# Kernel tuning notes

Hardware: AMD Instinct MI355X
Metric: run time of the kernel (lower is better)

The kernel has to match this reference:

```python
import jax, jax.numpy as jnp
import numpy as np

HID = 1024      # hidden_size (embedding dim, GRU input)
RNN = 1024      # rnn_hidden_size
VOCAB = 50000   # max_node
STEPS = 1024    # num_steps
SOS = 0


def setup_inputs() -> dict:
    key = jax.random.key(0)
    ks = jax.random.split(key, 8)
    s = 0.02
    return {
        "inputs": jax.random.randint(ks[0], (STEPS,), 0, VOCAB),
        "z": jax.random.normal(ks[1], (RNN,), jnp.float32),
        "emb_W": jax.random.uniform(ks[2], (VOCAB, HID), jnp.float32, -0.001, 0.001),
        "out_b": jnp.full((VOCAB,), 0.01, jnp.float32),
        "h2e_W": jax.random.normal(ks[3], (HID, RNN), jnp.float32) * s,
        "h2e_b": jnp.full((HID,), 0.01, jnp.float32),
        "W_ih": jax.random.normal(ks[4], (3 * RNN, HID), jnp.float32) * s,
        "W_hh": jax.random.normal(ks[5], (3 * RNN, RNN), jnp.float32) * s,
        "b_ih": jnp.zeros((3 * RNN,), jnp.float32),
        "b_hh": jnp.zeros((3 * RNN,), jnp.float32),
    }


def reference(inputs, z, emb_W, out_b, h2e_W, h2e_b, W_ih, W_hh, b_ih, b_hh):
    R = RNN

    def gru_cell(h, x):
        gi = W_ih @ x + b_ih          # (3R,)
        gh = W_hh @ h + b_hh          # (3R,)
        r = jax.nn.sigmoid(gi[:R] + gh[:R])
        zg = jax.nn.sigmoid(gi[R:2 * R] + gh[R:2 * R])
        n = jnp.tanh(gi[2 * R:] + r * gh[2 * R:])
        return (1.0 - zg) * n + zg * h

    # teacher forcing: step i consumes token_{i-1} (SOS for i=1), target is inputs[i]
    step_tokens = jnp.concatenate([jnp.array([SOS], dtype=inputs.dtype), inputs[1:-1]])
    targets = inputs[1:]

    def step(h, tok_tgt):
        tok, tgt = tok_tgt
        x = emb_W[tok]                              # embedding lookup (HID,)
        h_new = gru_cell(h, x)                      # (RNN,)
        e = h2e_W @ h_new + h2e_b                   # (HID,)
        logp = jax.nn.log_softmax(emb_W @ e + out_b)  # tied weights, (VOCAB,)
        return h_new, (-logp[tgt], jnp.argmax(logp))

    _, (losses, preds) = jax.lax.scan(step, z, (step_tokens, targets))
    loss = jnp.sum(losses)
    outputs = jnp.zeros((1, inputs.shape[0]), dtype=jnp.int32).at[0, 1:].set(preds.astype(jnp.int32))
    return loss, outputs
```

## Files before the change

kernel.cpp:

```cpp
#include <hip/hip_runtime.h>
#include <math.h>

#define NV      50000
#define T_STEPS 1023
#define KDIM    1024
#define NCH     782
typedef unsigned long long ull;


__global__ __launch_bounds__(256) void k_gather(const int* __restrict__ inputs,
                                                const float* __restrict__ emb,
                                                float* __restrict__ X) {
  const int t = blockIdx.x;
  const int tid = threadIdx.x;
  float4 v = make_float4(0.f, 0.f, 0.f, 0.f);
  if (t < T_STEPS) {
    const int tok = (t == 0) ? 0 : inputs[t];
    v = *(const float4*)&emb[(size_t)tok * KDIM + tid * 4];
  }
  *(float4*)&X[(size_t)t * KDIM + tid * 4] = v;
}

__global__ __launch_bounds__(256) void k_gemm_ffd(const float* __restrict__ A,
                                                  const float* __restrict__ B,
                                                  const float* __restrict__ bias,
                                                  double* __restrict__ C,
                                                  int N, int K) {
  __shared__ float As[32][68];
  __shared__ float Bs[32][68];
  const int tid = threadIdx.x;
  const int bx = blockIdx.x, by = blockIdx.y;
  const int lr = tid >> 2;
  const int lk = (tid & 3) * 8;
  const float* Ap = A + (size_t)(by * 64 + lr) * K + lk;
  const float* Bp = B + (size_t)(bx * 64 + lr) * K + lk;
  const int r0 = (tid >> 4) * 4;
  const int c0 = (tid & 15) * 4;
  double acc[4][4] = {};
  for (int kc = 0; kc < K; kc += 32) {
    const float4 a0 = *(const float4*)(Ap + kc);
    const float4 a1 = *(const float4*)(Ap + kc + 4);
    const float4 b0 = *(const float4*)(Bp + kc);
    const float4 b1 = *(const float4*)(Bp + kc + 4);
    __syncthreads();
    As[lk+0][lr]=a0.x; As[lk+1][lr]=a0.y; As[lk+2][lr]=a0.z; As[lk+3][lr]=a0.w;
    As[lk+4][lr]=a1.x; As[lk+5][lr]=a1.y; As[lk+6][lr]=a1.z; As[lk+7][lr]=a1.w;
    Bs[lk+0][lr]=b0.x; Bs[lk+1][lr]=b0.y; Bs[lk+2][lr]=b0.z; Bs[lk+3][lr]=b0.w;
    Bs[lk+4][lr]=b1.x; Bs[lk+5][lr]=b1.y; Bs[lk+6][lr]=b1.z; Bs[lk+7][lr]=b1.w;
    __syncthreads();
#pragma unroll
    for (int kk = 0; kk < 32; ++kk) {
      const float4 av = *(const float4*)&As[kk][r0];
      const float4 bv = *(const float4*)&Bs[kk][c0];
      const double aa[4] = {av.x, av.y, av.z, av.w};
      const double bb[4] = {bv.x, bv.y, bv.z, bv.w};
#pragma unroll
      for (int i = 0; i < 4; ++i)
#pragma unroll
        for (int j = 0; j < 4; ++j)
          acc[i][j] = fma(aa[i], bb[j], acc[i][j]);
    }
  }
  const int row = by * 64 + r0;
  const int col = bx * 64 + c0;
#pragma unroll
  for (int i = 0; i < 4; ++i)
#pragma unroll
    for (int j = 0; j < 4; ++j)
      C[(size_t)(row + i) * N + col + j] = acc[i][j] + (double)bias[col + j];
}

__global__ __launch_bounds__(256) void k_gemm_dfd(const double* __restrict__ A,
                                                  const float* __restrict__ B,
                                                  const float* __restrict__ bias,
                                                  double* __restrict__ C,
                                                  int N, int K) {
  __shared__ double As[32][68];
  __shared__ float  Bs[32][68];
  const int tid = threadIdx.x;
  const int bx = blockIdx.x, by = blockIdx.y;
  const int lr = tid >> 2;
  const int lk = (tid & 3) * 8;
  const double* Ap = A + (size_t)(by * 64 + lr) * K + lk;
  const float*  Bp = B + (size_t)(bx * 64 + lr) * K + lk;
  const int r0 = (tid >> 4) * 4;
  const int c0 = (tid & 15) * 4;
  double acc[4][4] = {};
  for (int kc = 0; kc < K; kc += 32) {
    double ar[8];
#pragma unroll
    for (int q = 0; q < 8; ++q) ar[q] = Ap[kc + q];
    const float4 b0 = *(const float4*)(Bp + kc);
    const float4 b1 = *(const float4*)(Bp + kc + 4);
    __syncthreads();
#pragma unroll
    for (int q = 0; q < 8; ++q) As[lk + q][lr] = ar[q];
    Bs[lk+0][lr]=b0.x; Bs[lk+1][lr]=b0.y; Bs[lk+2][lr]=b0.z; Bs[lk+3][lr]=b0.w;
    Bs[lk+4][lr]=b1.x; Bs[lk+5][lr]=b1.y; Bs[lk+6][lr]=b1.z; Bs[lk+7][lr]=b1.w;
    __syncthreads();
#pragma unroll
    for (int kk = 0; kk < 32; ++kk) {
      const double aa[4] = {As[kk][r0+0], As[kk][r0+1], As[kk][r0+2], As[kk][r0+3]};
      const float4 bv = *(const float4*)&Bs[kk][c0];
      const double bb[4] = {bv.x, bv.y, bv.z, bv.w};
#pragma unroll
      for (int i = 0; i < 4; ++i)
#pragma unroll
        for (int j = 0; j < 4; ++j)
          acc[i][j] = fma(aa[i], bb[j], acc[i][j]);
    }
  }
  const int row = by * 64 + r0;
  const int col = bx * 64 + c0;
#pragma unroll
  for (int i = 0; i < 4; ++i)
#pragma unroll
    for (int j = 0; j < 4; ++j)
      C[(size_t)(row + i) * N + col + j] = acc[i][j] + (double)bias[col + j];
}

__global__ __launch_bounds__(512, 2) void k_recur(const float* __restrict__ z,
                                                  const float* __restrict__ Whh,
                                                  const float* __restrict__ bhh,
                                                  const double* __restrict__ GI,
                                                  double* H, ull* SA, ull* SB,
                                                  int* done) {
  __shared__ double hs[1024];
  const int tid = threadIdx.x;
  const int w = tid >> 6, l = tid & 63;
  const int ibase = blockIdx.x * 16 + w * 2;
  float wreg[6][16];
#pragma unroll
  for (int il = 0; il < 2; ++il)
#pragma unroll
    for (int g = 0; g < 3; ++g) {
      const float* wp = Whh + (size_t)(g * 1024 + ibase + il) * 1024 + l;
#pragma unroll
      for (int m = 0; m < 16; ++m) wreg[il * 3 + g][m] = wp[m * 64];
    }
  double bh[6];
#pragma unroll
  for (int il = 0; il < 2; ++il)
#pragma unroll
    for (int g = 0; g < 3; ++g) bh[il * 3 + g] = (double)bhh[g * 1024 + ibase + il];

  hs[tid]       = (double)z[tid];
  hs[tid + 512] = (double)z[tid + 512];
  double gi[6];
#pragma unroll
  for (int il = 0; il < 2; ++il)
#pragma unroll
    for (int g = 0; g < 3; ++g) gi[il * 3 + g] = GI[g * 1024 + ibase + il];
  __syncthreads();

  for (int t = 0; t < T_STEPS; ++t) {
    const bool more = (t + 1 < T_STEPS);
    const int p = t & 1;
    const bool gate = more && (t >= 2);
    int dv = 0x7FFFFFFF;
    if (gate && tid < 64)
      dv = __hip_atomic_load(done + p * 64 + tid,
                             __ATOMIC_RELAXED, __HIP_MEMORY_SCOPE_AGENT);
    double s[6] = {0.0, 0.0, 0.0, 0.0, 0.0, 0.0};
#pragma unroll
    for (int m = 0; m < 16; ++m) {
      const double hv = hs[l + 64 * m];
#pragma unroll
      for (int rr = 0; rr < 6; ++rr) s[rr] = fma((double)wreg[rr][m], hv, s[rr]);
    }
#pragma unroll
    for (int rr = 0; rr < 6; ++rr) {
      double v = s[rr];
#pragma unroll
      for (int mk = 32; mk >= 1; mk >>= 1) v += __shfl_xor(v, mk, 64);
      s[rr] = v;
    }
    double hn = 0.0;
    if (l < 2) {
      const int il = l;
      const double r  = 1.0 / (1.0 + exp(-(gi[il * 3 + 0] + s[il * 3 + 0] + bh[il * 3 + 0])));
      const double zg = 1.0 / (1.0 + exp(-(gi[il * 3 + 1] + s[il * 3 + 1] + bh[il * 3 + 1])));
      const double n  = tanh(gi[il * 3 + 2] + r * (s[il * 3 + 2] + bh[il * 3 + 2]));
      hn = (1.0 - zg) * n + zg * hs[ibase + l];
    }
    double gin[6] = {0.0, 0.0, 0.0, 0.0, 0.0, 0.0};
    if (more) {
      const double* gp = GI + (size_t)(t + 1) * 3072;
#pragma unroll
      for (int il = 0; il < 2; ++il)
#pragma unroll
        for (int g = 0; g < 3; ++g) gin[il * 3 + g] = gp[g * 1024 + ibase + il];
    }
    if (gate && tid < 64) {
      while (!__all(dv >= t - 1)) {
        __builtin_amdgcn_s_sleep(1);
        dv = __hip_atomic_load(done + p * 64 + tid,
                               __ATOMIC_RELAXED, __HIP_MEMORY_SCOPE_AGENT);
      }
    }
    __syncthreads();
    if (l < 2) {
      const int gidx = ibase + l;
      __hip_atomic_store(H + (size_t)t * 1024 + gidx, hn,
                         __ATOMIC_RELAXED, __HIP_MEMORY_SCOPE_AGENT);
      if (more) {
        const ull hb  = (ull)__double_as_longlong(hn);
        const ull tag = ((ull)(t + 1)) << 32;
        __hip_atomic_store(SA + p * 1024 + gidx, tag | (hb >> 32),
                           __ATOMIC_RELAXED, __HIP_MEMORY_SCOPE_AGENT);
        __hip_atomic_store(SB + p * 1024 + gidx, tag | (hb & 0xFFFFFFFFull),
                           __ATOMIC_RELAXED, __HIP_MEMORY_SCOPE_AGENT);
      }
    }
    if (more) {
      const ull want = (ull)(t + 1);
      ull a0, b0, a1, b1;
      while (true) {
        a0 = __hip_atomic_load(SA + p * 1024 + tid,
                               __ATOMIC_RELAXED, __HIP_MEMORY_SCOPE_AGENT);
        b0 = __hip_atomic_load(SB + p * 1024 + tid,
                               __ATOMIC_RELAXED, __HIP_MEMORY_SCOPE_AGENT);
        if ((a0 >> 32) >= want && (b0 >> 32) >= want) break;
        __builtin_amdgcn_s_sleep(1);
      }
      while (true) {
        a1 = __hip_atomic_load(SA + p * 1024 + tid + 512,
                               __ATOMIC_RELAXED, __HIP_MEMORY_SCOPE_AGENT);
        b1 = __hip_atomic_load(SB + p * 1024 + tid + 512,
                               __ATOMIC_RELAXED, __HIP_MEMORY_SCOPE_AGENT);
        if ((a1 >> 32) >= want && (b1 >> 32) >= want) break;
        __builtin_amdgcn_s_sleep(1);
      }
      hs[tid]       = __longlong_as_double((long long)
                        (((a0 & 0xFFFFFFFFull) << 32) | (b0 & 0xFFFFFFFFull)));
      hs[tid + 512] = __longlong_as_double((long long)
                        (((a1 & 0xFFFFFFFFull) << 32) | (b1 & 0xFFFFFFFFull)));
      __syncthreads();
      if (tid == 0)
        __hip_atomic_store(done + p * 64 + blockIdx.x, t + 1,
                           __ATOMIC_RELAXED, __HIP_MEMORY_SCOPE_AGENT);
#pragma unroll
      for (int q = 0; q < 6; ++q) gi[q] = gin[q];
    }
  }
}

__global__ __launch_bounds__(256) void k_logits(const double* __restrict__ E,
                                                const float* __restrict__ emb,
                                                const float* __restrict__ out_b,
                                                const int* __restrict__ inputs,
                                                float* __restrict__ candL,
                                                int* __restrict__ candI,
                                                float* __restrict__ Psum,
                                                float* __restrict__ Ttgt) {
  __shared__ double As[32][68];
  __shared__ float  Bs[32][68];
  const int tid = threadIdx.x;
  const int bx = blockIdx.x, by = blockIdx.y;
  const int lr = tid >> 2;
  const int lk = (tid & 3) * 8;
  const int brow = bx * 64 + lr;
  const double* Ap = E + (size_t)(by * 64 + lr) * KDIM + lk;
  const float*  Bp = emb + (size_t)brow * KDIM + lk;
  const bool bvalid = (brow < NV);
  const int r0 = (tid >> 4) * 4;
  const int c0 = (tid & 15) * 4;
  double acc[4][4] = {};
  for (int kc = 0; kc < KDIM; kc += 32) {
    double ar[8];
#pragma unroll
    for (int q = 0; q < 8; ++q) ar[q] = Ap[kc + q];
    float4 b0 = make_float4(0.f, 0.f, 0.f, 0.f);
    float4 b1 = make_float4(0.f, 0.f, 0.f, 0.f);
    if (bvalid) { b0 = *(const float4*)(Bp + kc); b1 = *(const float4*)(Bp + kc + 4); }
    __syncthreads();
#pragma unroll
    for (int q = 0; q < 8; ++q) As[lk + q][lr] = ar[q];
    Bs[lk+0][lr]=b0.x; Bs[lk+1][lr]=b0.y; Bs[lk+2][lr]=b0.z; Bs[lk+3][lr]=b0.w;
    Bs[lk+4][lr]=b1.x; Bs[lk+5][lr]=b1.y; Bs[lk+6][lr]=b1.z; Bs[lk+7][lr]=b1.w;
    __syncthreads();
#pragma unroll
    for (int kk = 0; kk < 32; ++kk) {
      const double aa[4] = {As[kk][r0+0], As[kk][r0+1], As[kk][r0+2], As[kk][r0+3]};
      const float4 bv = *(const float4*)&Bs[kk][c0];
      const double bb[4] = {bv.x, bv.y, bv.z, bv.w};
#pragma unroll
      for (int i = 0; i < 4; ++i)
#pragma unroll
        for (int j = 0; j < 4; ++j)
          acc[i][j] = fma(aa[i], bb[j], acc[i][j]);
    }
  }
  const int colb = bx * 64 + c0;
#pragma unroll
  for (int i = 0; i < 4; ++i) {
    const int s = by * 64 + r0 + i;
    const bool valid = (s < T_STEPS);
    const int tgt = valid ? inputs[s + 1] : -1;
    float L1 = -3e38f, L2 = -3e38f;
    int   i1 = 0x7FFFFFFF, i2 = 0x7FFFFFFF;
    float se = 0.f, tv = -INFINITY;
#pragma unroll
    for (int j = 0; j < 4; ++j) {
      const int v = colb + j;
      if (v < NV) {
        const double lgd = acc[i][j] + (double)out_b[v];
        const float L = (float)lgd;
        se += expf((float)(lgd - 0.01));
        if (v == tgt) tv = (float)lgd;
        if (L > L1 || (L == L1 && v < i1)) { L2 = L1; i2 = i1; L1 = L; i1 = v; }
        else if (L > L2 || (L == L2 && v < i2)) { L2 = L; i2 = v; }
      }
    }
#pragma unroll
    for (int mk = 1; mk <= 8; mk <<= 1) {
      const float oL1 = __shfl_xor(L1, mk, 64); const int oi1 = __shfl_xor(i1, mk, 64);
      const float oL2 = __shfl_xor(L2, mk, 64); const int oi2 = __shfl_xor(i2, mk, 64);
      if (oL1 > L1 || (oL1 == L1 && oi1 < i1)) { L2 = L1; i2 = i1; L1 = oL1; i1 = oi1; }
      else if (oL1 > L2 || (oL1 == L2 && oi1 < i2)) { L2 = oL1; i2 = oi1; }
      if (oL2 > L1 || (oL2 == L1 && oi2 < i1)) { L2 = L1; i2 = i1; L1 = oL2; i1 = oi2; }
      else if (oL2 > L2 || (oL2 == L2 && oi2 < i2)) { L2 = oL2; i2 = oi2; }
      se += __shfl_xor(se, mk, 64);
      tv = fmaxf(tv, __shfl_xor(tv, mk, 64));
    }
    if (((tid & 15) == 0) && valid) {
      const size_t p = (size_t)s * (2 * NCH) + 2 * bx;
      candL[p] = L1;     candI[p] = i1;
      candL[p + 1] = L2; candI[p + 1] = i2;
      atomicAdd(&Psum[s], se);
      if (tv > -1e30f) Ttgt[s] = tv;
    }
  }
}

__global__ __launch_bounds__(256) void k_preds(const float* __restrict__ candL,
                                               const int* __restrict__ candI,
                                               float* __restrict__ out) {
  __shared__ float sL[256];
  __shared__ int   sI[256];
  const int s = blockIdx.x;
  const int tid = threadIdx.x;
  const int n = 2 * NCH;
  const size_t base = (size_t)s * n;
  float m = -3e38f;
  for (int c = tid; c < n; c += 256) m = fmaxf(m, candL[base + c]);
  sL[tid] = m; __syncthreads();
  for (int st = 128; st > 0; st >>= 1) {
    if (tid < st) sL[tid] = fmaxf(sL[tid], sL[tid + st]);
    __syncthreads();
  }
  const float Lmax = sL[0];
  __syncthreads();
  float bq = -3e38f; int bi = 0x7FFFFFFF;
  for (int c = tid; c < n; c += 256) {
    const float L = candL[base + c];
    const int   v = candI[base + c];
    const float d = L - Lmax;
    const float q = d - 10.8125f;
    if (q > bq || (q == bq && v < bi)) { bq = q; bi = v; }
  }
  sL[tid] = bq; sI[tid] = bi; __syncthreads();
  for (int st = 128; st > 0; st >>= 1) {
    if (tid < st) {
      if (sL[tid + st] > sL[tid] ||
          (sL[tid + st] == sL[tid] && sI[tid + st] < sI[tid])) {
        sL[tid] = sL[tid + st]; sI[tid] = sI[tid + st];
      }
    }
    __syncthreads();
  }
  if (tid == 0) out[2 + s] = (float)sI[0];
}

__global__ __launch_bounds__(1024) void k_finish(const float* __restrict__ Psum,
                                                 const float* __restrict__ Ttgt,
                                                 float* __restrict__ out) {
  __shared__ double red[1024];
  const int s = threadIdx.x;
  double ls = 0.0;
  if (s < T_STEPS) ls = 0.01 + log((double)Psum[s]) - (double)Ttgt[s];
  red[s] = ls;
  __syncthreads();
  for (int st = 512; st > 0; st >>= 1) {
    if (s < st) red[s] += red[s + st];
    __syncthreads();
  }
  if (s == 0) out[0] = (float)red[0];
  if (s == 1) out[1] = 0.f;
}

extern "C" void kernel_launch(void* const* d_in, const int* in_sizes, int n_in,
                              void* d_out, int out_size, void* d_ws, size_t ws_size,
                              hipStream_t stream) {
  const int*   inputs = (const int*)  d_in[0];
  const float* z      = (const float*)d_in[1];
  const float* emb    = (const float*)d_in[2];
  const float* out_b  = (const float*)d_in[3];
  const float* h2eW   = (const float*)d_in[4];
  const float* h2eb   = (const float*)d_in[5];
  const float* Wih    = (const float*)d_in[6];
  const float* Whh    = (const float*)d_in[7];
  const float* bih    = (const float*)d_in[8];
  const float* bhh    = (const float*)d_in[9];

  char* ws8 = (char*)d_ws;
  ull*    SA   = (ull*)ws8;
  ull*    SB   = (ull*)(ws8 + 16384);
  int*    done = (int*)(ws8 + 32768);
  float*  Psum = (float*)(ws8 + 33280);
  float*  Ttgt = (float*)(ws8 + 37376);
  float*  X    = (float*)(ws8 + 49152);
  char*   GIb  = ws8 + 49152 + (4u << 20);
  double* GI   = (double*)GIb;
  double* E    = GI;
  float*  candL = (float*)(GIb + (8u << 20));
  int*    candI = (int*)  (GIb + (8u << 20) + 6815744);
  double* H    = (double*)(ws8 + 49152 + (28u << 20));
  float*  out  = (float*)d_out;

  hipMemsetAsync(ws8, 0, 49152, stream);

  k_gather<<<1024, 256, 0, stream>>>(inputs, emb, X);
  k_gemm_ffd<<<dim3(48, 16), 256, 0, stream>>>(X, Wih, bih, GI, 3072, KDIM);
  k_recur<<<64, 512, 0, stream>>>(z, Whh, bhh, GI, H, SA, SB, done);
  k_gemm_dfd<<<dim3(16, 16), 256, 0, stream>>>(H, h2eW, h2eb, E, KDIM, KDIM);
  k_logits<<<dim3(NCH, 16), 256, 0, stream>>>(E, emb, out_b, inputs,
                                              candL, candI, Psum, Ttgt);
  k_preds<<<T_STEPS, 256, 0, stream>>>(candL, candI, out);
  k_finish<<<1, 1024, 0, stream>>>(Psum, Ttgt, out);
}
```

Measured before the change: 9.355 ms.

## Widen logits tile, deepen recurrence slot ring, and merge spin-wait loops

The logits GEMM tile grows from 64 to 128 vocab columns per block, so each thread holds a 4x8 double accumulator and the number of column chunks halves. This improves reuse of the E operand at the cost of more registers. The GRU recurrence now cycles through 4 handoff slots instead of 2, which loosens the done-gating between blocks. Its two separate spin loops become one, and the H store becomes a plain store. Workspace offsets are enlarged to fit the bigger slot arrays.

After: 9.260 ms. No clear change (-1.0%).

```diff
diff --git a/kernel.cpp b/kernel.cpp
--- a/kernel.cpp
+++ b/kernel.cpp
@@ -4,7 +4,7 @@
 #define NV      50000
 #define T_STEPS 1023
 #define KDIM    1024
-#define NCH     782
+#define NCH     391
 typedef unsigned long long ull;
 
 
@@ -123,8 +123,8 @@
                                                   const float* __restrict__ Whh,
                                                   const float* __restrict__ bhh,
                                                   const double* __restrict__ GI,
-                                                  double* H, ull* SA, ull* SB,
-                                                  int* done) {
+                                                  double* __restrict__ H,
+                                                  ull* SA, ull* SB, int* done) {
   __shared__ double hs[1024];
   const int tid = threadIdx.x;
   const int w = tid >> 6, l = tid & 63;
@@ -155,8 +155,8 @@
 
   for (int t = 0; t < T_STEPS; ++t) {
     const bool more = (t + 1 < T_STEPS);
-    const int p = t & 1;
-    const bool gate = more && (t >= 2);
+    const int p = t & 3;
+    const bool gate = more && (t >= 4);
     int dv = 0x7FFFFFFF;
     if (gate && tid < 64)
       dv = __hip_atomic_load(done + p * 64 + tid,
@@ -192,7 +192,7 @@
         for (int g = 0; g < 3; ++g) gin[il * 3 + g] = gp[g * 1024 + ibase + il];
     }
     if (gate && tid < 64) {
-      while (!__all(dv >= t - 1)) {
+      while (!__all(dv >= t - 3)) {
         __builtin_amdgcn_s_sleep(1);
         dv = __hip_atomic_load(done + p * 64 + tid,
                                __ATOMIC_RELAXED, __HIP_MEMORY_SCOPE_AGENT);
@@ -201,8 +201,7 @@
     __syncthreads();
     if (l < 2) {
       const int gidx = ibase + l;
-      __hip_atomic_store(H + (size_t)t * 1024 + gidx, hn,
-                         __ATOMIC_RELAXED, __HIP_MEMORY_SCOPE_AGENT);
+      H[(size_t)t * 1024 + gidx] = hn;
       if (more) {
         const ull hb  = (ull)__double_as_longlong(hn);
         const ull tag = ((ull)(t + 1)) << 32;
@@ -220,15 +219,12 @@
                                __ATOMIC_RELAXED, __HIP_MEMORY_SCOPE_AGENT);
         b0 = __hip_atomic_load(SB + p * 1024 + tid,
                                __ATOMIC_RELAXED, __HIP_MEMORY_SCOPE_AGENT);
-        if ((a0 >> 32) >= want && (b0 >> 32) >= want) break;
-        __builtin_amdgcn_s_sleep(1);
-      }
-      while (true) {
         a1 = __hip_atomic_load(SA + p * 1024 + tid + 512,
                                __ATOMIC_RELAXED, __HIP_MEMORY_SCOPE_AGENT);
         b1 = __hip_atomic_load(SB + p * 1024 + tid + 512,
                                __ATOMIC_RELAXED, __HIP_MEMORY_SCOPE_AGENT);
-        if ((a1 >> 32) >= want && (b1 >> 32) >= want) break;
+        if ((a0 >> 32) >= want && (b0 >> 32) >= want &&
+            (a1 >> 32) >= want && (b1 >> 32) >= want) break;
         __builtin_amdgcn_s_sleep(1);
       }
       hs[tid]       = __longlong_as_double((long long)
@@ -253,45 +249,56 @@
                                                 int* __restrict__ candI,
                                                 float* __restrict__ Psum,
                                                 float* __restrict__ Ttgt) {
-  __shared__ double As[32][68];
-  __shared__ float  Bs[32][68];
+  __shared__ double As[32][66];
+  __shared__ float  Bs[32][132];
   const int tid = threadIdx.x;
   const int bx = blockIdx.x, by = blockIdx.y;
   const int lr = tid >> 2;
   const int lk = (tid & 3) * 8;
-  const int brow = bx * 64 + lr;
   const double* Ap = E + (size_t)(by * 64 + lr) * KDIM + lk;
-  const float*  Bp = emb + (size_t)brow * KDIM + lk;
+  const int bcol = tid >> 1;
+  const int bk   = (tid & 1) * 16;
+  const int brow = bx * 128 + bcol;
+  const float* Bp = emb + (size_t)brow * KDIM + bk;
   const bool bvalid = (brow < NV);
   const int r0 = (tid >> 4) * 4;
-  const int c0 = (tid & 15) * 4;
-  double acc[4][4] = {};
+  const int c0 = (tid & 15) * 8;
+  double acc[4][8] = {};
   for (int kc = 0; kc < KDIM; kc += 32) {
     double ar[8];
 #pragma unroll
     for (int q = 0; q < 8; ++q) ar[q] = Ap[kc + q];
-    float4 b0 = make_float4(0.f, 0.f, 0.f, 0.f);
-    float4 b1 = make_float4(0.f, 0.f, 0.f, 0.f);
-    if (bvalid) { b0 = *(const float4*)(Bp + kc); b1 = *(const float4*)(Bp + kc + 4); }
+    float4 br[4];
+#pragma unroll
+    for (int q = 0; q < 4; ++q)
+      br[q] = bvalid ? *(const float4*)(Bp + kc + q * 4)
+                     : make_float4(0.f, 0.f, 0.f, 0.f);
     __syncthreads();
 #pragma unroll
     for (int q = 0; q < 8; ++q) As[lk + q][lr] = ar[q];
-    Bs[lk+0][lr]=b0.x; Bs[lk+1][lr]=b0.y; Bs[lk+2][lr]=b0.z; Bs[lk+3][lr]=b0.w;
-    Bs[lk+4][lr]=b1.x; Bs[lk+5][lr]=b1.y; Bs[lk+6][lr]=b1.z; Bs[lk+7][lr]=b1.w;
+#pragma unroll
+    for (int q = 0; q < 4; ++q) {
+      Bs[bk + q * 4 + 0][bcol] = br[q].x;
+      Bs[bk + q * 4 + 1][bcol] = br[q].y;
+      Bs[bk + q * 4 + 2][bcol] = br[q].z;
+      Bs[bk + q * 4 + 3][bcol] = br[q].w;
+    }
     __syncthreads();
 #pragma unroll
     for (int kk = 0; kk < 32; ++kk) {
       const double aa[4] = {As[kk][r0+0], As[kk][r0+1], As[kk][r0+2], As[kk][r0+3]};
-      const float4 bv = *(const float4*)&Bs[kk][c0];
-      const double bb[4] = {bv.x, bv.y, bv.z, bv.w};
+      const float4 bv0 = *(const float4*)&Bs[kk][c0];
+      const float4 bv1 = *(const float4*)&Bs[kk][c0 + 4];
+      const double bb[8] = {bv0.x, bv0.y, bv0.z, bv0.w,
+                            bv1.x, bv1.y, bv1.z, bv1.w};
 #pragma unroll
       for (int i = 0; i < 4; ++i)
 #pragma unroll
-        for (int j = 0; j < 4; ++j)
+        for (int j = 0; j < 8; ++j)
           acc[i][j] = fma(aa[i], bb[j], acc[i][j]);
     }
   }
-  const int colb = bx * 64 + c0;
+  const int colb = bx * 128 + c0;
 #pragma unroll
   for (int i = 0; i < 4; ++i) {
     const int s = by * 64 + r0 + i;
@@ -301,7 +308,7 @@
     int   i1 = 0x7FFFFFFF, i2 = 0x7FFFFFFF;
     float se = 0.f, tv = -INFINITY;
 #pragma unroll
-    for (int j = 0; j < 4; ++j) {
+    for (int j = 0; j < 8; ++j) {
       const int v = colb + j;
       if (v < NV) {
         const double lgd = acc[i][j] + (double)out_b[v];
@@ -405,20 +412,20 @@
 
   char* ws8 = (char*)d_ws;
   ull*    SA   = (ull*)ws8;
-  ull*    SB   = (ull*)(ws8 + 16384);
-  int*    done = (int*)(ws8 + 32768);
-  float*  Psum = (float*)(ws8 + 33280);
-  float*  Ttgt = (float*)(ws8 + 37376);
-  float*  X    = (float*)(ws8 + 49152);
-  char*   GIb  = ws8 + 49152 + (4u << 20);
+  ull*    SB   = (ull*)(ws8 + 32768);
+  int*    done = (int*)(ws8 + 65536);
+  float*  Psum = (float*)(ws8 + 66560);
+  float*  Ttgt = (float*)(ws8 + 70656);
+  float*  X    = (float*)(ws8 + 81920);
+  char*   GIb  = ws8 + 81920 + (4u << 20);
   double* GI   = (double*)GIb;
   double* E    = GI;
   float*  candL = (float*)(GIb + (8u << 20));
-  int*    candI = (int*)  (GIb + (8u << 20) + 6815744);
-  double* H    = (double*)(ws8 + 49152 + (28u << 20));
+  int*    candI = (int*)  (GIb + (8u << 20) + 3211264);
+  double* H    = (double*)(ws8 + 81920 + (28u << 20));
   float*  out  = (float*)d_out;
 
-  hipMemsetAsync(ws8, 0, 49152, stream);
+  hipMemsetAsync(ws8, 0, 81920, stream);
 
   k_gather<<<1024, 256, 0, stream>>>(inputs, emb, X);
   k_gemm_ffd<<<dim3(48, 16), 256, 0, stream>>>(X, Wih, bih, GI, 3072, KDIM);
```
